# Performance work log

Measured on AMD Instinct MI355X. Metric: run time of the kernel, lower is better.

Reference implementation:

```python
import jax, jax.numpy as jnp
import numpy as np

EPSILON = 1e-05


def setup_inputs() -> dict:
    key = jax.random.key(0)
    k1, k2, k3 = jax.random.split(key, 3)
    B, T, D, K = 8, 4096, 256, 2048
    hidden_states = jax.random.normal(k1, (B, T, D), dtype=jnp.float32)
    embed_sum = jax.random.normal(k2, (K, D), dtype=jnp.float32)
    # cluster usage counts are positive in practice
    cluster_usage = jax.random.uniform(k3, (K,), dtype=jnp.float32) * 10.0 + 0.1
    return {
        "hidden_states": hidden_states,
        "embed_sum": embed_sum,
        "cluster_usage": cluster_usage,
    }


def reference(hidden_states, embed_sum, cluster_usage):
    # embed = embed_sum / clamp(cluster_usage, eps)   -> [K, D]
    embed = embed_sum / jnp.clip(cluster_usage, EPSILON, None)[:, None]

    shape = hidden_states.shape
    x = hidden_states.reshape(-1, shape[-1])  # [N, D]

    # squared L2 distances via norm expansion (argmin equals argmin of cdist p=2)
    x_sq = jnp.sum(x * x, axis=-1, keepdims=True)          # [N, 1]
    e_sq = jnp.sum(embed * embed, axis=-1)[None, :]         # [1, K]
    dots = jnp.einsum("nd,kd->nk", x, embed)               # [N, K]
    dists = x_sq - 2.0 * dots + e_sq                        # [N, K]

    embed_ind = jnp.argmin(dists, axis=-1)                 # [N]
    embed_ind = embed_ind.reshape(shape[:-1])              # [B, T]

    # decode: embedding lookup
    quantize = embed[embed_ind]                             # [B, T, D]
    return quantize, embed_ind
```

## Files before the change

kernel.cpp:

```cpp
#include <hip/hip_runtime.h>
#include <float.h>
#include <stdint.h>


#define EPSILON 1e-5f
#define DELTA   1e-3f

constexpr int D     = 256;
constexpr int K_TOT = 2048;

constexpr int RES_H      = 16384;
constexpr int ESQ_H      = 32768;
constexpr int LDS_HALVES = 36864;
constexpr int DYN_LDS    = LDS_HALVES * 2;

typedef _Float16 half8v  __attribute__((ext_vector_type(8)));
typedef _Float16 half4v  __attribute__((ext_vector_type(4)));
typedef float    f32x4   __attribute__((ext_vector_type(4)));

#define GLL(SRC, DST)                                                   \
  __builtin_amdgcn_global_load_lds(                                     \
      (const __attribute__((address_space(1))) void*)(SRC),             \
      (__attribute__((address_space(3))) void*)(DST), 16, 0, 0)

__global__ void prep_kernel(const float* __restrict__ es,
                            const float* __restrict__ usage,
                            _Float16* __restrict__ ec,
                            float* __restrict__ esq,
                            int* __restrict__ counter) {
  const int bx   = blockIdx.x;
  const int t    = threadIdx.x;
  const int wid  = t >> 6;
  const int lane = t & 63;
  if (bx < K_TOT / 4) {
    const int k = bx * 4 + wid;
    const float u = fmaxf(usage[k], EPSILON);
    const float4 v = *(const float4*)(es + (size_t)k * D + lane * 4);
    float4 e;
    e.x = v.x / u; e.y = v.y / u; e.z = v.z / u; e.w = v.w / u;
    half4v h, lo;
    h.x = (_Float16)e.x; lo.x = (_Float16)(e.x - (float)h.x);
    h.y = (_Float16)e.y; lo.y = (_Float16)(e.y - (float)h.y);
    h.z = (_Float16)e.z; lo.z = (_Float16)(e.z - (float)h.z);
    h.w = (_Float16)e.w; lo.w = (_Float16)(e.w - (float)h.w);
    *(half4v*)(ec + (size_t)k * 512 + lane * 4)       = h;
    *(half4v*)(ec + (size_t)k * 512 + 256 + lane * 4) = lo;
    float s = e.x * e.x + e.y * e.y + e.z * e.z + e.w * e.w;
    #pragma unroll
    for (int m = 1; m < 64; m <<= 1) s += __shfl_xor(s, m, 64);
    if (lane == 0) esq[k] = s;
  } else {
    if (t == 0) *counter = 0;
  }
}

__global__ __launch_bounds__(256, 2)
void mm_kernel(const float* __restrict__ x, const _Float16* __restrict__ ec,
               const float* __restrict__ esq, const float* __restrict__ es,
               const float* __restrict__ usage,
               float* __restrict__ out_q, float* __restrict__ out_i,
               int* __restrict__ list, int* __restrict__ counter,
               unsigned long long* __restrict__ rmin, int N) {
  extern __shared__ __align__(16) _Float16 lds[];
  const int t    = threadIdx.x;
  const int lane = t & 63;
  const int q    = lane >> 4;
  const int l15  = lane & 15;
  const int wid  = t >> 6;
  const int wn   = wid >> 1;
  const int wk   = wid & 1;
  const int n0   = blockIdx.x * 64;

  float* esq_lds = (float*)&lds[ESQ_H];
  {
    *(float4*)&esq_lds[t * 8]     = *(const float4*)(esq + t * 8);
    *(float4*)&esq_lds[t * 8 + 4] = *(const float4*)(esq + t * 8 + 4);
  }

  const int prow  = t >> 2;
  const int pc    = t & 3;
  const int wbase = (t >> 6) * 512 + ((t & 63) ^ ((t >> 3) & 3)) * 8;
  #pragma unroll
  for (int i = 0; i < 8; ++i) {
    const float* src = x + (size_t)(n0 + prow) * D + i * 32 + pc * 8;
    const float4 f0 = *(const float4*)src;
    const float4 f1 = *(const float4*)(src + 4);
    const float f[8] = {f0.x, f0.y, f0.z, f0.w, f1.x, f1.y, f1.z, f1.w};
    half8v hv, lv;
    #pragma unroll
    for (int e = 0; e < 8; ++e) {
      const _Float16 h = (_Float16)f[e];
      hv[e] = h;
      lv[e] = (_Float16)(f[e] - (float)h);
    }
    *(half8v*)&lds[i * 2048 + wbase]         = hv;
    *(half8v*)&lds[RES_H + i * 2048 + wbase] = lv;
  }
  __syncthreads();

  const int gA = l15 * 4 + q;
  const int sp = (gA ^ ((l15 >> 1) & 3)) * 8;

  half8v ahr[8][2];
  #pragma unroll
  for (int s = 0; s < 8; ++s)
    #pragma unroll
    for (int mi = 0; mi < 2; ++mi)
      ahr[s][mi] = *(const half8v*)
          &lds[s * 2048 + (wn * 2 + mi) * 512 + sp];
  __syncthreads();

  const int r0 = t >> 3;
  const int cl = (t & 7) ^ (r0 & 7);
  const _Float16* pB = ec + (size_t)r0 * 512 + cl * 8;

  #pragma unroll
  for (int i = 0; i < 4; ++i)
    GLL(pB + i * 16384, &lds[i * 2048 + t * 8]);

  int bfoff[4][2];
  #pragma unroll
  for (int ni = 0; ni < 4; ++ni)
    #pragma unroll
    for (int j = 0; j < 2; ++j)
      bfoff[ni][j] = (wk * 64 + ni * 16 + l15) * 64 +
                     (((j << 2) + q) ^ (l15 & 7)) * 8;

  float rd0[2][4], rd1[2][4];
  int   ri0[2][4];
  #pragma unroll
  for (int mi = 0; mi < 2; ++mi)
    #pragma unroll
    for (int r = 0; r < 4; ++r) {
      rd0[mi][r] = FLT_MAX; rd1[mi][r] = FLT_MAX; ri0[mi][r] = 0x7fffffff;
    }

  for (int kt = 0; kt < 16; ++kt) {
    int   kc[4];
    float eqv[4];
    #pragma unroll
    for (int ni = 0; ni < 4; ++ni) {
      kc[ni]  = kt * 128 + wk * 64 + ni * 16 + l15;
      eqv[ni] = esq_lds[kc[ni]];
    }

    f32x4 acc[2][4] = {};

    #pragma unroll
    for (int sidx = 0; sidx < 8; ++sidx) {
      const int ss = kt * 8 + sidx;
      asm volatile("s_waitcnt vmcnt(0)" ::: "memory");
      __builtin_amdgcn_s_barrier();
      __builtin_amdgcn_sched_barrier(0);

      if (ss < 127) {
        const int ns = ss + 1;
        const _Float16* np = pB + (size_t)(ns >> 3) * 65536 + (ns & 7) * 64;
        const int nb = (ns & 1) * 8192;
        #pragma unroll
        for (int i = 0; i < 4; ++i)
          GLL(np + i * 16384, &lds[nb + i * 2048 + t * 8]);
      }

      const int bb = (ss & 1) * 8192;
      __builtin_amdgcn_s_setprio(1);
      #pragma unroll
      for (int j = 0; j < 2; ++j) {
        half8v bf[4];
        #pragma unroll
        for (int ni = 0; ni < 4; ++ni)
          bf[ni] = *(const half8v*)&lds[bb + bfoff[ni][j]];
        const int ks = (sidx & 3) * 2 + j;
        if (sidx < 4) {
          half8v al[2];
          #pragma unroll
          for (int mi = 0; mi < 2; ++mi)
            al[mi] = *(const half8v*)
                &lds[RES_H + ks * 2048 + (wn * 2 + mi) * 512 + sp];
          #pragma unroll
          for (int mi = 0; mi < 2; ++mi)
            #pragma unroll
            for (int ni = 0; ni < 4; ++ni)
              acc[mi][ni] = __builtin_amdgcn_mfma_f32_16x16x32_f16(
                  ahr[ks][mi], bf[ni], acc[mi][ni], 0, 0, 0);
          #pragma unroll
          for (int mi = 0; mi < 2; ++mi)
            #pragma unroll
            for (int ni = 0; ni < 4; ++ni)
              acc[mi][ni] = __builtin_amdgcn_mfma_f32_16x16x32_f16(
                  al[mi], bf[ni], acc[mi][ni], 0, 0, 0);
        } else {
          #pragma unroll
          for (int mi = 0; mi < 2; ++mi)
            #pragma unroll
            for (int ni = 0; ni < 4; ++ni)
              acc[mi][ni] = __builtin_amdgcn_mfma_f32_16x16x32_f16(
                  ahr[ks][mi], bf[ni], acc[mi][ni], 0, 0, 0);
        }
      }
      __builtin_amdgcn_s_setprio(0);
    }

    #pragma unroll
    for (int ni = 0; ni < 4; ++ni) {
      #pragma unroll
      for (int mi = 0; mi < 2; ++mi) {
        #pragma unroll
        for (int r = 0; r < 4; ++r) {
          const float d = fmaf(-2.f, acc[mi][ni][r], eqv[ni]);
          if (d < rd0[mi][r]) {
            rd1[mi][r] = rd0[mi][r]; rd0[mi][r] = d; ri0[mi][r] = kc[ni];
          } else {
            rd1[mi][r] = fminf(rd1[mi][r], d);
          }
        }
      }
    }
  }
  __syncthreads();

  float* ex = (float*)lds;
  #pragma unroll
  for (int mi = 0; mi < 2; ++mi) {
    #pragma unroll
    for (int r = 0; r < 4; ++r) {
      float d0 = rd0[mi][r], d1 = rd1[mi][r];
      int   i0 = ri0[mi][r];
      #pragma unroll
      for (int off = 1; off < 16; off <<= 1) {
        const float od0 = __shfl_xor(d0, off, 16);
        const int   oi0 = __shfl_xor(i0, off, 16);
        const float od1 = __shfl_xor(d1, off, 16);
        if (od0 < d0 || (od0 == d0 && oi0 < i0)) {
          d1 = fminf(d0, od1); d0 = od0; i0 = oi0;
        } else {
          d1 = fminf(d1, od0);
        }
      }
      if (l15 == mi * 8 + r) {
        const int row = wn * 32 + mi * 16 + q * 4 + r;
        *(float4*)&ex[(row * 2 + wk) * 4] =
            make_float4(d0, __int_as_float(i0), d1, 0.f);
      }
    }
  }
  __syncthreads();

  {
    const int row = t >> 2;
    const int seg = t & 3;
    const float4 a = *(const float4*)&ex[(row * 2 + 0) * 4];
    const float4 b = *(const float4*)&ex[(row * 2 + 1) * 4];
    float d0, d1; int i0;
    const int ia = __float_as_int(a.y), ib = __float_as_int(b.y);
    if (b.x < a.x || (b.x == a.x && ib < ia)) {
      d0 = b.x; i0 = ib; d1 = fminf(a.x, b.z);
    } else {
      d0 = a.x; i0 = ia; d1 = fminf(a.z, b.x);
    }
    const int n = n0 + row;
    const float u  = fmaxf(usage[i0], EPSILON);
    const float4* src = (const float4*)(es + (size_t)i0 * D);
    float4*       dst = (float4*)(out_q + (size_t)n * D);
    #pragma unroll
    for (int i = 0; i < 16; ++i) {
      const int j = i * 4 + seg;
      const float4 e = src[j];
      dst[j] = make_float4(e.x / u, e.y / u, e.z / u, e.w / u);
    }
    if (seg == 0) {
      out_i[n] = (float)i0;
      if (d1 - d0 < DELTA) {
        rmin[n] = 0xFFFFFFFFFFFFFFFFull;
        const int pos = atomicAdd(counter, 1);
        list[pos] = n;
      }
    }
  }
}

__global__ void repair_kernel(const float* __restrict__ x,
                              const float* __restrict__ es,
                              const float* __restrict__ usage,
                              const float* __restrict__ esq,
                              const int* __restrict__ list,
                              const int* __restrict__ counter,
                              unsigned long long* __restrict__ rmin) {
  __shared__ float xs[256];
  const int t    = threadIdx.x;
  const int w    = t >> 6;
  const int lane = t & 63;
  const int cnt  = *counter;
  const int kseg = blockIdx.x & 7;

  for (int j = blockIdx.x >> 3; j < cnt; j += 256) {
    const int n = list[j];
    __syncthreads();
    xs[t] = x[(size_t)n * D + t];
    __syncthreads();
    const float4 xv = *(const float4*)&xs[lane * 4];

    float bd = FLT_MAX;
    int   bi = 0x7fffffff;
    const int kb0 = kseg * 256 + w * 64;
    for (int kk = 0; kk < 64; kk += 4) {
      const int kbase = kb0 + kk;
      float pd[4];
      #pragma unroll
      for (int j2 = 0; j2 < 4; ++j2) {
        const int k = kbase + j2;
        const float rs = 1.0f / fmaxf(usage[k], EPSILON);
        const float4 e = *(const float4*)(es + (size_t)k * D + lane * 4);
        float p = xv.x * (e.x * rs);
        p = fmaf(xv.y, e.y * rs, p);
        p = fmaf(xv.z, e.z * rs, p);
        pd[j2] = fmaf(xv.w, e.w * rs, p);
      }
      #pragma unroll
      for (int off = 1; off < 64; off <<= 1) {
        pd[0] += __shfl_xor(pd[0], off, 64);
        pd[1] += __shfl_xor(pd[1], off, 64);
        pd[2] += __shfl_xor(pd[2], off, 64);
        pd[3] += __shfl_xor(pd[3], off, 64);
      }
      #pragma unroll
      for (int j2 = 0; j2 < 4; ++j2) {
        const float dst = fmaf(-2.f, pd[j2], esq[kbase + j2]);
        if (dst < bd) { bd = dst; bi = kbase + j2; }
      }
    }
    if (lane == 0) {
      uint32_t ub = __float_as_uint(bd);
      ub = (ub & 0x80000000u) ? ~ub : (ub | 0x80000000u);
      const unsigned long long pk =
          ((unsigned long long)ub << 32) | (unsigned)bi;
      atomicMin(&rmin[n], pk);
    }
  }
}

__global__ void repair2_kernel(const float* __restrict__ es,
                               const float* __restrict__ usage,
                               const int* __restrict__ list,
                               const int* __restrict__ counter,
                               const unsigned long long* __restrict__ rmin,
                               float* __restrict__ out_q,
                               float* __restrict__ out_i) {
  const int t   = threadIdx.x;
  const int cnt = *counter;
  for (int j = blockIdx.x; j < cnt; j += 1024) {
    const int n   = list[j];
    const int idx = (int)(rmin[n] & 0x7fffffffu);
    const float u = fmaxf(usage[idx], EPSILON);
    out_q[(size_t)n * D + t] = es[(size_t)idx * D + t] / u;
    if (t == 0) out_i[n] = (float)idx;
  }
}

constexpr int TN = 128;
constexpr int DC = 32;
constexpr int KS = 2;
constexpr int RS = 196;

__global__ void esq_kernel(const float* __restrict__ es,
                           const float* __restrict__ usage,
                           float* __restrict__ esq) {
  const int lane = threadIdx.x & 63;
  const int w    = threadIdx.x >> 6;
  const int k    = blockIdx.x * 4 + w;
  const float u  = fmaxf(usage[k], EPSILON);
  const float4 e = *(const float4*)(es + (size_t)k * D + lane * 4);
  const float a = e.x / u, b = e.y / u, c = e.z / u, d = e.w / u;
  float s = a * a + b * b + c * c + d * d;
  #pragma unroll
  for (int m = 1; m < 64; m <<= 1) s += __shfl_xor(s, m, 64);
  if (lane == 0) esq[k] = s;
}

__global__ __launch_bounds__(256, 2)
void dist_kernel(const float* __restrict__ x,
                 const float* __restrict__ es,
                 const float* __restrict__ usage,
                 const float* __restrict__ esq,
                 float* __restrict__ bestd,
                 int* __restrict__ besti, int N) {
  __shared__ float smX[DC * RS];
  __shared__ float smE[DC * RS];
  const int t    = threadIdx.x;
  const int tx   = t & 15;
  const int ty   = t >> 4;
  const int n0   = blockIdx.x * TN;
  const int half = blockIdx.y;

  float best[8];
  int   bidx[8];
  #pragma unroll
  for (int i = 0; i < 8; ++i) { best[i] = FLT_MAX; bidx[i] = 0; }

  for (int kt = 0; kt < (K_TOT / KS) / 128; ++kt) {
    const int k0 = half * (K_TOT / KS) + kt * 128;
    float acc[8][8];
    #pragma unroll
    for (int i = 0; i < 8; ++i)
      #pragma unroll
      for (int j = 0; j < 8; ++j) acc[i][j] = 0.f;

    for (int dc = 0; dc < D; dc += DC) {
      __syncthreads();
      #pragma unroll
      for (int i = 0; i < 4; ++i) {
        const int f    = i * 256 + t;
        const int row  = f >> 3;
        const int c4   = f & 7;
        const int pcol = row + ((row >> 3) << 2);
        const float4 xv =
            *(const float4*)(x + (size_t)(n0 + row) * D + dc + c4 * 4);
        smX[(c4 * 4 + 0) * RS + pcol] = xv.x;
        smX[(c4 * 4 + 1) * RS + pcol] = xv.y;
        smX[(c4 * 4 + 2) * RS + pcol] = xv.z;
        smX[(c4 * 4 + 3) * RS + pcol] = xv.w;
        const int kk = k0 + row;
        const float rs = 1.0f / fmaxf(usage[kk], EPSILON);
        const float4 ev =
            *(const float4*)(es + (size_t)kk * D + dc + c4 * 4);
        smE[(c4 * 4 + 0) * RS + pcol] = ev.x * rs;
        smE[(c4 * 4 + 1) * RS + pcol] = ev.y * rs;
        smE[(c4 * 4 + 2) * RS + pcol] = ev.z * rs;
        smE[(c4 * 4 + 3) * RS + pcol] = ev.w * rs;
      }
      __syncthreads();
      #pragma unroll 4
      for (int d = 0; d < DC; ++d) {
        const float* px = &smX[d * RS + ty * 12];
        const float* pe = &smE[d * RS + tx * 12];
        const float4 xa = *(const float4*)px;
        const float4 xb = *(const float4*)(px + 4);
        const float4 ea = *(const float4*)pe;
        const float4 eb = *(const float4*)(pe + 4);
        const float xr[8] = {xa.x, xa.y, xa.z, xa.w, xb.x, xb.y, xb.z, xb.w};
        const float er[8] = {ea.x, ea.y, ea.z, ea.w, eb.x, eb.y, eb.z, eb.w};
        #pragma unroll
        for (int i = 0; i < 8; ++i)
          #pragma unroll
          for (int jj = 0; jj < 8; ++jj)
            acc[i][jj] = fmaf(xr[i], er[jj], acc[i][jj]);
      }
    }
    #pragma unroll
    for (int jj = 0; jj < 8; ++jj) {
      const int k = k0 + tx * 8 + jj;
      const float eq = esq[k];
      #pragma unroll
      for (int i = 0; i < 8; ++i) {
        const float dst = fmaf(-2.0f, acc[i][jj], eq);
        if (dst < best[i]) { best[i] = dst; bidx[i] = k; }
      }
    }
  }
  __syncthreads();
  float* rd = smX;
  int*   ri = (int*)smE;
  #pragma unroll
  for (int i = 0; i < 8; ++i) {
    const int r = ty * 8 + i;
    rd[tx * TN + r] = best[i];
    ri[tx * TN + r] = bidx[i];
  }
  __syncthreads();
  for (int off = 8; off >= 1; off >>= 1) {
    if (tx < off) {
      #pragma unroll
      for (int i = 0; i < 8; ++i) {
        const int r = ty * 8 + i;
        const float da = rd[tx * TN + r], db = rd[(tx + off) * TN + r];
        const int   ia = ri[tx * TN + r], ib = ri[(tx + off) * TN + r];
        if (db < da || (db == da && ib < ia)) {
          rd[tx * TN + r] = db;
          ri[tx * TN + r] = ib;
        }
      }
    }
    __syncthreads();
  }
  if (tx == 0) {
    #pragma unroll
    for (int i = 0; i < 8; ++i) {
      const int r = ty * 8 + i;
      bestd[(size_t)half * N + n0 + r] = rd[r];
      besti[(size_t)half * N + n0 + r] = ri[r];
    }
  }
}

__global__ void gather_kernel(const float* __restrict__ es,
                              const float* __restrict__ usage,
                              const float* __restrict__ bestd,
                              const int* __restrict__ besti,
                              float* __restrict__ out_q,
                              float* __restrict__ out_i, int N) {
  const int w    = threadIdx.x >> 6;
  const int lane = threadIdx.x & 63;
  const int n    = blockIdx.x * 4 + w;
  const float d0 = bestd[n];
  const float d1 = bestd[(size_t)N + n];
  const int   i0 = besti[n];
  const int   i1 = besti[(size_t)N + n];
  const int idx = (d1 < d0) ? i1 : i0;
  const float u = fmaxf(usage[idx], EPSILON);
  const float4 e = *(const float4*)(es + (size_t)idx * D + lane * 4);
  float4 qv;
  qv.x = e.x / u; qv.y = e.y / u; qv.z = e.z / u; qv.w = e.w / u;
  *(float4*)(out_q + (size_t)n * D + lane * 4) = qv;
  if (lane == 0) out_i[n] = (float)idx;
}

extern "C" void kernel_launch(void* const* d_in, const int* in_sizes, int n_in,
                              void* d_out, int out_size, void* d_ws, size_t ws_size,
                              hipStream_t stream) {
  const float* x     = (const float*)d_in[0];
  const float* es    = (const float*)d_in[1];
  const float* usage = (const float*)d_in[2];
  const int N = in_sizes[0] / D;

  float* out_q = (float*)d_out;
  float* out_i = out_q + (size_t)N * D;

  const size_t EB = (size_t)K_TOT * 512 * 2;
  const size_t off_esq  = EB;
  const size_t off_list = off_esq + 8192;
  const size_t off_cnt  = off_list + (size_t)N * 4;
  const size_t off_rmin = off_cnt + 16;
  const size_t NEED     = off_rmin + (size_t)N * 8;

  char* wsb = (char*)d_ws;

  hipError_t attr_ok = hipFuncSetAttribute(
      (const void*)mm_kernel, hipFuncAttributeMaxDynamicSharedMemorySize,
      DYN_LDS);

  if (ws_size >= NEED && attr_ok == hipSuccess && (N % 64) == 0) {
    _Float16* ec   = (_Float16*)wsb;
    float*    esq  = (float*)(wsb + off_esq);
    int*      list = (int*)(wsb + off_list);
    int*      cnt  = (int*)(wsb + off_cnt);
    unsigned long long* rmin = (unsigned long long*)(wsb + off_rmin);

    prep_kernel<<<K_TOT / 4 + 1, 256, 0, stream>>>(es, usage, ec, esq, cnt);
    mm_kernel<<<N / 64, 256, DYN_LDS, stream>>>(x, ec, esq, es, usage,
                                                out_q, out_i, list, cnt,
                                                rmin, N);
    repair_kernel<<<2048, 256, 0, stream>>>(x, es, usage, esq, list, cnt, rmin);
    repair2_kernel<<<1024, 256, 0, stream>>>(es, usage, list, cnt, rmin,
                                             out_q, out_i);
  } else {
    float* ws    = (float*)d_ws;
    float* esq   = ws;
    float* bestd = ws + K_TOT;
    int*   besti = (int*)(ws + K_TOT + (size_t)KS * N);
    esq_kernel<<<K_TOT / 4, 256, 0, stream>>>(es, usage, esq);
    dist_kernel<<<dim3(N / TN, KS), 256, 0, stream>>>(x, es, usage, esq,
                                                      bestd, besti, N);
    gather_kernel<<<N / 4, 256, 0, stream>>>(es, usage, bestd, besti,
                                             out_q, out_i, N);
  }
}
```

Before: 189.6 us.

## Split codebook across two blocks per row tile and add combine kernel

The matmul kernel now splits the 2048-entry codebook into two halves, each handled by its own block, doubling the grid. Each block writes its partial top-2 distances to a workspace buffer, and a new combine kernel merges them and does the gather, output write and ambiguity flagging. The residual A fragments move from LDS into registers, which shrinks LDS so occupancy can rise to 3 blocks per CU. In exchange the x tile is loaded and split twice, there is an extra kernel launch with a global round trip, and register pressure rises.

```diff
diff --git a/kernel.cpp b/kernel.cpp
--- a/kernel.cpp
+++ b/kernel.cpp
@@ -9,9 +9,8 @@
 constexpr int D     = 256;
 constexpr int K_TOT = 2048;
 
-constexpr int RES_H      = 16384;
-constexpr int ESQ_H      = 32768;
-constexpr int LDS_HALVES = 36864;
+constexpr int ESQ_H      = 16384;
+constexpr int LDS_HALVES = 18432;
 constexpr int DYN_LDS    = LDS_HALVES * 2;
 
 typedef _Float16 half8v  __attribute__((ext_vector_type(8)));
@@ -54,13 +53,9 @@
   }
 }
 
-__global__ __launch_bounds__(256, 2)
+__global__ __launch_bounds__(256, 3)
 void mm_kernel(const float* __restrict__ x, const _Float16* __restrict__ ec,
-               const float* __restrict__ esq, const float* __restrict__ es,
-               const float* __restrict__ usage,
-               float* __restrict__ out_q, float* __restrict__ out_i,
-               int* __restrict__ list, int* __restrict__ counter,
-               unsigned long long* __restrict__ rmin, int N) {
+               const float* __restrict__ esq, float4* __restrict__ p4, int N) {
   extern __shared__ __align__(16) _Float16 lds[];
   const int t    = threadIdx.x;
   const int lane = t & 63;
@@ -69,50 +64,55 @@
   const int wid  = t >> 6;
   const int wn   = wid >> 1;
   const int wk   = wid & 1;
-  const int n0   = blockIdx.x * 64;
+  const int nb   = blockIdx.x >> 1;
+  const int kb   = blockIdx.x & 1;
+  const int n0   = nb * 64;
 
   float* esq_lds = (float*)&lds[ESQ_H];
-  {
-    *(float4*)&esq_lds[t * 8]     = *(const float4*)(esq + t * 8);
-    *(float4*)&esq_lds[t * 8 + 4] = *(const float4*)(esq + t * 8 + 4);
-  }
+  *(float4*)&esq_lds[t * 4] = *(const float4*)(esq + kb * 1024 + t * 4);
 
   const int prow  = t >> 2;
   const int pc    = t & 3;
   const int wbase = (t >> 6) * 512 + ((t & 63) ^ ((t >> 3) & 3)) * 8;
-  #pragma unroll
-  for (int i = 0; i < 8; ++i) {
-    const float* src = x + (size_t)(n0 + prow) * D + i * 32 + pc * 8;
-    const float4 f0 = *(const float4*)src;
-    const float4 f1 = *(const float4*)(src + 4);
-    const float f[8] = {f0.x, f0.y, f0.z, f0.w, f1.x, f1.y, f1.z, f1.w};
-    half8v hv, lv;
-    #pragma unroll
-    for (int e = 0; e < 8; ++e) {
-      const _Float16 h = (_Float16)f[e];
-      hv[e] = h;
-      lv[e] = (_Float16)(f[e] - (float)h);
-    }
-    *(half8v*)&lds[i * 2048 + wbase]         = hv;
-    *(half8v*)&lds[RES_H + i * 2048 + wbase] = lv;
-  }
-  __syncthreads();
-
   const int gA = l15 * 4 + q;
   const int sp = (gA ^ ((l15 >> 1) & 3)) * 8;
 
-  half8v ahr[8][2];
-  #pragma unroll
-  for (int s = 0; s < 8; ++s)
-    #pragma unroll
-    for (int mi = 0; mi < 2; ++mi)
-      ahr[s][mi] = *(const half8v*)
-          &lds[s * 2048 + (wn * 2 + mi) * 512 + sp];
-  __syncthreads();
+  half8v ahr[8][2], alr[8][2];
+  #pragma unroll
+  for (int h = 0; h < 2; ++h) {
+    #pragma unroll
+    for (int i = 0; i < 4; ++i) {
+      const int rg = h * 4 + i;
+      const float* src = x + (size_t)(n0 + prow) * D + rg * 32 + pc * 8;
+      const float4 f0 = *(const float4*)src;
+      const float4 f1 = *(const float4*)(src + 4);
+      const float f[8] = {f0.x, f0.y, f0.z, f0.w, f1.x, f1.y, f1.z, f1.w};
+      half8v hv, lv;
+      #pragma unroll
+      for (int e = 0; e < 8; ++e) {
+        const _Float16 hh = (_Float16)f[e];
+        hv[e] = hh;
+        lv[e] = (_Float16)(f[e] - (float)hh);
+      }
+      *(half8v*)&lds[i * 2048 + wbase]        = hv;
+      *(half8v*)&lds[8192 + i * 2048 + wbase] = lv;
+    }
+    __syncthreads();
+    #pragma unroll
+    for (int i = 0; i < 4; ++i)
+      #pragma unroll
+      for (int mi = 0; mi < 2; ++mi) {
+        ahr[h * 4 + i][mi] = *(const half8v*)
+            &lds[i * 2048 + (wn * 2 + mi) * 512 + sp];
+        alr[h * 4 + i][mi] = *(const half8v*)
+            &lds[8192 + i * 2048 + (wn * 2 + mi) * 512 + sp];
+      }
+    __syncthreads();
+  }
 
   const int r0 = t >> 3;
   const int cl = (t & 7) ^ (r0 & 7);
-  const _Float16* pB = ec + (size_t)r0 * 512 + cl * 8;
+  const _Float16* pB = ec + (size_t)(kb * 1024 + r0) * 512 + cl * 8;
 
   #pragma unroll
   for (int i = 0; i < 4; ++i)
@@ -135,13 +135,14 @@
       rd0[mi][r] = FLT_MAX; rd1[mi][r] = FLT_MAX; ri0[mi][r] = 0x7fffffff;
     }
 
-  for (int kt = 0; kt < 16; ++kt) {
+  for (int kt = 0; kt < 8; ++kt) {
     int   kc[4];
     float eqv[4];
     #pragma unroll
     for (int ni = 0; ni < 4; ++ni) {
-      kc[ni]  = kt * 128 + wk * 64 + ni * 16 + l15;
-      eqv[ni] = esq_lds[kc[ni]];
+      const int kl = kt * 128 + wk * 64 + ni * 16 + l15;
+      kc[ni]  = kb * 1024 + kl;
+      eqv[ni] = esq_lds[kl];
     }
 
     f32x4 acc[2][4] = {};
@@ -153,13 +154,13 @@
       __builtin_amdgcn_s_barrier();
       __builtin_amdgcn_sched_barrier(0);
 
-      if (ss < 127) {
+      if (ss < 63) {
         const int ns = ss + 1;
         const _Float16* np = pB + (size_t)(ns >> 3) * 65536 + (ns & 7) * 64;
-        const int nb = (ns & 1) * 8192;
+        const int nbuf = (ns & 1) * 8192;
         #pragma unroll
         for (int i = 0; i < 4; ++i)
-          GLL(np + i * 16384, &lds[nb + i * 2048 + t * 8]);
+          GLL(np + i * 16384, &lds[nbuf + i * 2048 + t * 8]);
       }
 
       const int bb = (ss & 1) * 8192;
@@ -172,11 +173,6 @@
           bf[ni] = *(const half8v*)&lds[bb + bfoff[ni][j]];
         const int ks = (sidx & 3) * 2 + j;
         if (sidx < 4) {
-          half8v al[2];
-          #pragma unroll
-          for (int mi = 0; mi < 2; ++mi)
-            al[mi] = *(const half8v*)
-                &lds[RES_H + ks * 2048 + (wn * 2 + mi) * 512 + sp];
           #pragma unroll
           for (int mi = 0; mi < 2; ++mi)
             #pragma unroll
@@ -188,7 +184,7 @@
             #pragma unroll
             for (int ni = 0; ni < 4; ++ni)
               acc[mi][ni] = __builtin_amdgcn_mfma_f32_16x16x32_f16(
-                  al[mi], bf[ni], acc[mi][ni], 0, 0, 0);
+                  alr[ks][mi], bf[ni], acc[mi][ni], 0, 0, 0);
         } else {
           #pragma unroll
           for (int mi = 0; mi < 2; ++mi)
@@ -217,9 +213,7 @@
       }
     }
   }
-  __syncthreads();
-
-  float* ex = (float*)lds;
+
   #pragma unroll
   for (int mi = 0; mi < 2; ++mi) {
     #pragma unroll
@@ -239,42 +233,57 @@
       }
       if (l15 == mi * 8 + r) {
         const int row = wn * 32 + mi * 16 + q * 4 + r;
-        *(float4*)&ex[(row * 2 + wk) * 4] =
+        p4[(size_t)(n0 + row) * 4 + kb * 2 + wk] =
             make_float4(d0, __int_as_float(i0), d1, 0.f);
       }
     }
   }
-  __syncthreads();
-
-  {
-    const int row = t >> 2;
-    const int seg = t & 3;
-    const float4 a = *(const float4*)&ex[(row * 2 + 0) * 4];
-    const float4 b = *(const float4*)&ex[(row * 2 + 1) * 4];
-    float d0, d1; int i0;
-    const int ia = __float_as_int(a.y), ib = __float_as_int(b.y);
-    if (b.x < a.x || (b.x == a.x && ib < ia)) {
-      d0 = b.x; i0 = ib; d1 = fminf(a.x, b.z);
+}
+
+__global__ void combine_kernel(const float4* __restrict__ p4,
+                               const float* __restrict__ es,
+                               const float* __restrict__ usage,
+                               float* __restrict__ out_q,
+                               float* __restrict__ out_i,
+                               int* __restrict__ list,
+                               int* __restrict__ counter,
+                               unsigned long long* __restrict__ rmin, int N) {
+  const int wid  = threadIdx.x >> 6;
+  const int lane = threadIdx.x & 63;
+  const int n    = blockIdx.x * 4 + wid;
+
+  float d0 = FLT_MAX, d1 = FLT_MAX;
+  int   i0 = 0x7fffffff;
+  if (lane < 4) {
+    const float4 pv = p4[(size_t)n * 4 + lane];
+    d0 = pv.x; i0 = __float_as_int(pv.y); d1 = pv.z;
+  }
+  #pragma unroll
+  for (int off = 1; off < 4; off <<= 1) {
+    const float od0 = __shfl_xor(d0, off, 4);
+    const int   oi0 = __shfl_xor(i0, off, 4);
+    const float od1 = __shfl_xor(d1, off, 4);
+    if (od0 < d0 || (od0 == d0 && oi0 < i0)) {
+      d1 = fminf(d0, od1); d0 = od0; i0 = oi0;
     } else {
-      d0 = a.x; i0 = ia; d1 = fminf(a.z, b.x);
-    }
-    const int n = n0 + row;
-    const float u  = fmaxf(usage[i0], EPSILON);
-    const float4* src = (const float4*)(es + (size_t)i0 * D);
-    float4*       dst = (float4*)(out_q + (size_t)n * D);
-    #pragma unroll
-    for (int i = 0; i < 16; ++i) {
-      const int j = i * 4 + seg;
-      const float4 e = src[j];
-      dst[j] = make_float4(e.x / u, e.y / u, e.z / u, e.w / u);
-    }
-    if (seg == 0) {
-      out_i[n] = (float)i0;
-      if (d1 - d0 < DELTA) {
-        rmin[n] = 0xFFFFFFFFFFFFFFFFull;
-        const int pos = atomicAdd(counter, 1);
-        list[pos] = n;
-      }
+      d1 = fminf(d1, od0);
+    }
+  }
+  const int   idx = __shfl(i0, 0, 64);
+  const float g0  = __shfl(d0, 0, 64);
+  const float g1  = __shfl(d1, 0, 64);
+
+  const float u = fmaxf(usage[idx], EPSILON);
+  const float4 e = *(const float4*)(es + (size_t)idx * D + lane * 4);
+  float4 qv;
+  qv.x = e.x / u; qv.y = e.y / u; qv.z = e.z / u; qv.w = e.w / u;
+  *(float4*)(out_q + (size_t)n * D + lane * 4) = qv;
+  if (lane == 0) {
+    out_i[n] = (float)idx;
+    if (g1 - g0 < DELTA) {
+      rmin[n] = 0xFFFFFFFFFFFFFFFFull;
+      const int pos = atomicAdd(counter, 1);
+      list[pos] = n;
     }
   }
 }
@@ -526,7 +535,9 @@
   float* out_i = out_q + (size_t)N * D;
 
   const size_t EB = (size_t)K_TOT * 512 * 2;
-  const size_t off_esq  = EB;
+  const size_t PB = (size_t)N * 4 * 16;
+  const size_t off_p4   = EB;
+  const size_t off_esq  = off_p4 + PB;
   const size_t off_list = off_esq + 8192;
   const size_t off_cnt  = off_list + (size_t)N * 4;
   const size_t off_rmin = off_cnt + 16;
@@ -540,15 +551,16 @@
 
   if (ws_size >= NEED && attr_ok == hipSuccess && (N % 64) == 0) {
     _Float16* ec   = (_Float16*)wsb;
+    float4*   p4   = (float4*)(wsb + off_p4);
     float*    esq  = (float*)(wsb + off_esq);
     int*      list = (int*)(wsb + off_list);
     int*      cnt  = (int*)(wsb + off_cnt);
     unsigned long long* rmin = (unsigned long long*)(wsb + off_rmin);
 
     prep_kernel<<<K_TOT / 4 + 1, 256, 0, stream>>>(es, usage, ec, esq, cnt);
-    mm_kernel<<<N / 64, 256, DYN_LDS, stream>>>(x, ec, esq, es, usage,
-                                                out_q, out_i, list, cnt,
-                                                rmin, N);
+    mm_kernel<<<(N / 64) * 2, 256, DYN_LDS, stream>>>(x, ec, esq, p4, N);
+    combine_kernel<<<N / 4, 256, 0, stream>>>(p4, es, usage, out_q, out_i,
+                                              list, cnt, rmin, N);
     repair_kernel<<<2048, 256, 0, stream>>>(x, es, usage, esq, list, cnt, rmin);
     repair2_kernel<<<1024, 256, 0, stream>>>(es, usage, list, cnt, rmin,
                                              out_q, out_i);
```

Result: slower. 261.7 us (+38.0%).

## Split mm_kernel K-tile across 8 waves instead of 4

Applied to the files above, without the earlier changes.

Doubles the block to 512 threads so each wave handles 32 codebook columns instead of 64 per K-tile. Staging loads, B-fragment offsets, the partial-result exchange and the final four-way merge are all rewritten for the new wave split. The aim is more waves in flight per block to hide LDS and MFMA latency, and less accumulator register pressure per wave. The cost is more barrier participants and less MFMA work between each synchronisation. Occupancy is still bounded by LDS, and launch_bounds(512,4) may force register limits that cause spills.

```diff
diff --git a/kernel.cpp b/kernel.cpp
--- a/kernel.cpp
+++ b/kernel.cpp
@@ -54,7 +54,7 @@
   }
 }
 
-__global__ __launch_bounds__(256, 2)
+__global__ __launch_bounds__(512, 4)
 void mm_kernel(const float* __restrict__ x, const _Float16* __restrict__ ec,
                const float* __restrict__ esq, const float* __restrict__ es,
                const float* __restrict__ usage,
@@ -67,22 +67,22 @@
   const int q    = lane >> 4;
   const int l15  = lane & 15;
   const int wid  = t >> 6;
-  const int wn   = wid >> 1;
-  const int wk   = wid & 1;
+  const int wn   = wid >> 2;
+  const int wk   = wid & 3;
   const int n0   = blockIdx.x * 64;
 
   float* esq_lds = (float*)&lds[ESQ_H];
-  {
-    *(float4*)&esq_lds[t * 8]     = *(const float4*)(esq + t * 8);
-    *(float4*)&esq_lds[t * 8 + 4] = *(const float4*)(esq + t * 8 + 4);
-  }
-
-  const int prow  = t >> 2;
-  const int pc    = t & 3;
-  const int wbase = (t >> 6) * 512 + ((t & 63) ^ ((t >> 3) & 3)) * 8;
-  #pragma unroll
-  for (int i = 0; i < 8; ++i) {
-    const float* src = x + (size_t)(n0 + prow) * D + i * 32 + pc * 8;
+  *(float4*)&esq_lds[t * 4] = *(const float4*)(esq + t * 4);
+
+  const int tt    = t & 255;
+  const int rgn   = t >> 8;
+  const int prow  = tt >> 2;
+  const int pc    = tt & 3;
+  const int wbase = (tt >> 6) * 512 + ((tt & 63) ^ ((tt >> 3) & 3)) * 8;
+  #pragma unroll
+  for (int i = 0; i < 4; ++i) {
+    const int rg = i * 2 + rgn;
+    const float* src = x + (size_t)(n0 + prow) * D + rg * 32 + pc * 8;
     const float4 f0 = *(const float4*)src;
     const float4 f1 = *(const float4*)(src + 4);
     const float f[8] = {f0.x, f0.y, f0.z, f0.w, f1.x, f1.y, f1.z, f1.w};
@@ -93,8 +93,8 @@
       hv[e] = h;
       lv[e] = (_Float16)(f[e] - (float)h);
     }
-    *(half8v*)&lds[i * 2048 + wbase]         = hv;
-    *(half8v*)&lds[RES_H + i * 2048 + wbase] = lv;
+    *(half8v*)&lds[rg * 2048 + wbase]         = hv;
+    *(half8v*)&lds[RES_H + rg * 2048 + wbase] = lv;
   }
   __syncthreads();
 
@@ -114,16 +114,15 @@
   const int cl = (t & 7) ^ (r0 & 7);
   const _Float16* pB = ec + (size_t)r0 * 512 + cl * 8;
 
-  #pragma unroll
-  for (int i = 0; i < 4; ++i)
-    GLL(pB + i * 16384, &lds[i * 2048 + t * 8]);
-
-  int bfoff[4][2];
-  #pragma unroll
-  for (int ni = 0; ni < 4; ++ni)
+  GLL(pB,         &lds[t * 8]);
+  GLL(pB + 32768, &lds[4096 + t * 8]);
+
+  int bfoff[2][2];
+  #pragma unroll
+  for (int ni = 0; ni < 2; ++ni)
     #pragma unroll
     for (int j = 0; j < 2; ++j)
-      bfoff[ni][j] = (wk * 64 + ni * 16 + l15) * 64 +
+      bfoff[ni][j] = (wk * 32 + ni * 16 + l15) * 64 +
                      (((j << 2) + q) ^ (l15 & 7)) * 8;
 
   float rd0[2][4], rd1[2][4];
@@ -136,15 +135,15 @@
     }
 
   for (int kt = 0; kt < 16; ++kt) {
-    int   kc[4];
-    float eqv[4];
-    #pragma unroll
-    for (int ni = 0; ni < 4; ++ni) {
-      kc[ni]  = kt * 128 + wk * 64 + ni * 16 + l15;
+    int   kc[2];
+    float eqv[2];
+    #pragma unroll
+    for (int ni = 0; ni < 2; ++ni) {
+      kc[ni]  = kt * 128 + wk * 32 + ni * 16 + l15;
       eqv[ni] = esq_lds[kc[ni]];
     }
 
-    f32x4 acc[2][4] = {};
+    f32x4 acc[2][2] = {};
 
     #pragma unroll
     for (int sidx = 0; sidx < 8; ++sidx) {
@@ -157,18 +156,17 @@
         const int ns = ss + 1;
         const _Float16* np = pB + (size_t)(ns >> 3) * 65536 + (ns & 7) * 64;
         const int nb = (ns & 1) * 8192;
-        #pragma unroll
-        for (int i = 0; i < 4; ++i)
-          GLL(np + i * 16384, &lds[nb + i * 2048 + t * 8]);
+        GLL(np,         &lds[nb + t * 8]);
+        GLL(np + 32768, &lds[nb + 4096 + t * 8]);
       }
 
       const int bb = (ss & 1) * 8192;
       __builtin_amdgcn_s_setprio(1);
       #pragma unroll
       for (int j = 0; j < 2; ++j) {
-        half8v bf[4];
+        half8v bf[2];
         #pragma unroll
-        for (int ni = 0; ni < 4; ++ni)
+        for (int ni = 0; ni < 2; ++ni)
           bf[ni] = *(const half8v*)&lds[bb + bfoff[ni][j]];
         const int ks = (sidx & 3) * 2 + j;
         if (sidx < 4) {
@@ -180,20 +178,20 @@
           #pragma unroll
           for (int mi = 0; mi < 2; ++mi)
             #pragma unroll
-            for (int ni = 0; ni < 4; ++ni)
+            for (int ni = 0; ni < 2; ++ni)
               acc[mi][ni] = __builtin_amdgcn_mfma_f32_16x16x32_f16(
                   ahr[ks][mi], bf[ni], acc[mi][ni], 0, 0, 0);
           #pragma unroll
           for (int mi = 0; mi < 2; ++mi)
             #pragma unroll
-            for (int ni = 0; ni < 4; ++ni)
+            for (int ni = 0; ni < 2; ++ni)
               acc[mi][ni] = __builtin_amdgcn_mfma_f32_16x16x32_f16(
                   al[mi], bf[ni], acc[mi][ni], 0, 0, 0);
         } else {
           #pragma unroll
           for (int mi = 0; mi < 2; ++mi)
             #pragma unroll
-            for (int ni = 0; ni < 4; ++ni)
+            for (int ni = 0; ni < 2; ++ni)
               acc[mi][ni] = __builtin_amdgcn_mfma_f32_16x16x32_f16(
                   ahr[ks][mi], bf[ni], acc[mi][ni], 0, 0, 0);
         }
@@ -202,7 +200,7 @@
     }
 
     #pragma unroll
-    for (int ni = 0; ni < 4; ++ni) {
+    for (int ni = 0; ni < 2; ++ni) {
       #pragma unroll
       for (int mi = 0; mi < 2; ++mi) {
         #pragma unroll
@@ -239,7 +237,7 @@
       }
       if (l15 == mi * 8 + r) {
         const int row = wn * 32 + mi * 16 + q * 4 + r;
-        *(float4*)&ex[(row * 2 + wk) * 4] =
+        *(float4*)&ex[(row * 4 + wk) * 4] =
             make_float4(d0, __int_as_float(i0), d1, 0.f);
       }
     }
@@ -247,24 +245,27 @@
   __syncthreads();
 
   {
-    const int row = t >> 2;
-    const int seg = t & 3;
-    const float4 a = *(const float4*)&ex[(row * 2 + 0) * 4];
-    const float4 b = *(const float4*)&ex[(row * 2 + 1) * 4];
-    float d0, d1; int i0;
-    const int ia = __float_as_int(a.y), ib = __float_as_int(b.y);
-    if (b.x < a.x || (b.x == a.x && ib < ia)) {
-      d0 = b.x; i0 = ib; d1 = fminf(a.x, b.z);
-    } else {
-      d0 = a.x; i0 = ia; d1 = fminf(a.z, b.x);
+    const int row = t >> 3;
+    const int seg = t & 7;
+    float d0 = FLT_MAX, d1 = FLT_MAX;
+    int   i0 = 0x7fffffff;
+    #pragma unroll
+    for (int p = 0; p < 4; ++p) {
+      const float4 pv = *(const float4*)&ex[(row * 4 + p) * 4];
+      const int    pi = __float_as_int(pv.y);
+      if (pv.x < d0 || (pv.x == d0 && pi < i0)) {
+        d1 = fminf(d0, pv.z); d0 = pv.x; i0 = pi;
+      } else {
+        d1 = fminf(d1, pv.x);
+      }
     }
     const int n = n0 + row;
     const float u  = fmaxf(usage[i0], EPSILON);
     const float4* src = (const float4*)(es + (size_t)i0 * D);
     float4*       dst = (float4*)(out_q + (size_t)n * D);
     #pragma unroll
-    for (int i = 0; i < 16; ++i) {
-      const int j = i * 4 + seg;
+    for (int ii = 0; ii < 8; ++ii) {
+      const int j = ii * 8 + seg;
       const float4 e = src[j];
       dst[j] = make_float4(e.x / u, e.y / u, e.z / u, e.w / u);
     }
@@ -546,7 +547,7 @@
     unsigned long long* rmin = (unsigned long long*)(wsb + off_rmin);
 
     prep_kernel<<<K_TOT / 4 + 1, 256, 0, stream>>>(es, usage, ec, esq, cnt);
-    mm_kernel<<<N / 64, 256, DYN_LDS, stream>>>(x, ec, esq, es, usage,
+    mm_kernel<<<N / 64, 512, DYN_LDS, stream>>>(x, ec, esq, es, usage,
                                                 out_q, out_i, list, cnt,
                                                 rmin, N);
     repair_kernel<<<2048, 256, 0, stream>>>(x, es, usage, esq, list, cnt, rmin);
```

Result: slower. 232.9 us (+22.8%).
